# Optimization experiments

Hardware: AMD Instinct MI355X
Metric: run time of the kernel (lower is better)

The kernel has to match this reference:

```python
import jax, jax.numpy as jnp
import numpy as np

NUM_ITERS = 5
EPS = 1e-5


def setup_inputs() -> dict:
    key = jax.random.key(0)
    ks = jax.random.split(key, 5)
    C_in, C_out, D, H, W = 64, 64, 64, 256, 256
    return {
        "x": jax.random.normal(ks[0], (C_in, H, W), dtype=jnp.float32),
        "conv_w": jax.random.normal(ks[1], (C_out, C_in, 3, 3), dtype=jnp.float32) * 0.05,
        "conv_b": jax.random.normal(ks[2], (C_out,), dtype=jnp.float32) * 0.05,
        "bin_proj": jax.random.normal(ks[3], (C_out, D, 1), dtype=jnp.float32),
        "weight_matrix": jax.random.normal(ks[4], (C_out, D, D), dtype=jnp.float32),
        "gn_weight": jnp.ones((C_out,), dtype=jnp.float32),
        "gn_bias": jnp.zeros((C_out,), dtype=jnp.float32),
    }


def reference(x, conv_w, conv_b, bin_proj, weight_matrix, gn_weight, gn_bias):
    # query conv: (C_in,H,W) -> (C_out,H,W), SAME padding
    q = jax.lax.conv_general_dilated(
        x[None], conv_w, window_strides=(1, 1), padding="SAME",
        dimension_numbers=("NCHW", "OIHW", "NCHW"))[0]
    q = q + conv_b[:, None, None]

    bp = bin_proj[:, :, 0]  # (C, D) == bin_proj_c[:, 0] per channel
    # binary query / initial state: (C, H, W, D)
    state = jnp.sign(q[:, :, :, None] * bp[:, None, None, :])
    # unrolled Hopfield dynamics: state = sign(W_c @ state) per channel/pixel
    for _ in range(NUM_ITERS):
        state = jnp.sign(jnp.einsum("cde,chwe->chwd", weight_matrix, state))
    # readout: sum_d bp[c,d] * state[c,h,w,d] -> (C,H,W)
    out = jnp.einsum("cd,chwd->chw", bp, state)

    # GroupNorm(groups=1) over (C,H,W) with per-channel affine, then residual input is out+q
    y = out + q
    mean = jnp.mean(y)
    var = jnp.mean(jnp.square(y - mean))
    yn = (y - mean) * jax.lax.rsqrt(var + EPS)
    yn = yn * gn_weight[:, None, None] + gn_bias[:, None, None]
    return jax.nn.gelu(yn)
```

## Files before the change

kernel.cpp:

```cpp
#include <hip/hip_runtime.h>
#include <math.h>

#define N_TOT 4194304
#define CONV_BLOCKS 1024
#define XS_PAD 4864

__device__ __forceinline__ float sgnf(float x) {
    return x > 0.f ? 1.f : (x < 0.f ? -1.f : 0.f);
}

__device__ __forceinline__ float gelu_f(float v) {
    const float c0 = 0.7978845608028654f;
    float inner = c0 * fmaf(0.044715f * v, v * v, v);
    return 0.5f * v * (1.f + tanhf(inner));
}

__device__ __forceinline__ void gll4(const float* g, float* l) {
    __builtin_amdgcn_global_load_lds((const __attribute__((address_space(1))) void*)g,
                                     (__attribute__((address_space(3))) void*)l, 4, 0, 0);
}

__global__ __launch_bounds__(64) void alpha_kernel(const float* __restrict__ bp,
                                                   const float* __restrict__ Wm,
                                                   float* __restrict__ alpha) {
    const int c = blockIdx.x, d = threadIdx.x;
    __shared__ float v[64];
    float bpv = bp[c * 64 + d];
    v[d] = sgnf(bpv);
    __syncthreads();
    const float* row = Wm + c * 4096 + d * 64;
    for (int it = 0; it < 5; ++it) {
        float s = 0.f;
        #pragma unroll
        for (int e = 0; e < 64; ++e) s = fmaf(row[e], v[e], s);
        __syncthreads();
        v[d] = sgnf(s);
        __syncthreads();
    }
    float val = bpv * v[d];
    #pragma unroll
    for (int off = 32; off; off >>= 1) val += __shfl_down(val, off);
    if (d == 0) alpha[c] = val;
}

#define LOAD_T(T, XSC, CIOFF)                                                 \
    {                                                                         \
        _Pragma("unroll")                                                     \
        for (int rr = 0; rr < 4; ++rr) {                                      \
            const int off_ = lrow + rr * 136 + (CIOFF);                       \
            float2 a_ = *reinterpret_cast<const float2*>(&(XSC)[off_]);       \
            float2 b_ = *reinterpret_cast<const float2*>(&(XSC)[off_ + 2]);   \
            T[rr][0] = a_.x; T[rr][1] = a_.y; T[rr][2] = b_.x; T[rr][3] = b_.y;\
        }                                                                     \
    }

#define FMA_CI(T, WP)                                                         \
    {                                                                         \
        _Pragma("unroll")                                                     \
        for (int co = 0; co < 4; ++co) {                                      \
            const float* w_ = (WP) + co * 576;                                \
            _Pragma("unroll")                                                 \
            for (int ky = 0; ky < 3; ++ky)                                    \
                _Pragma("unroll")                                             \
                for (int kx = 0; kx < 3; ++kx) {                              \
                    float wv_ = w_[ky * 3 + kx];                              \
                    _Pragma("unroll")                                         \
                    for (int dy = 0; dy < 2; ++dy)                            \
                        _Pragma("unroll")                                     \
                        for (int j = 0; j < 2; ++j)                           \
                            acc[co][dy][j] = fmaf(wv_, T[dy + ky][kx + j],    \
                                                  acc[co][dy][j]);            \
                }                                                             \
        }                                                                     \
    }

__global__ __launch_bounds__(256, 2) void conv_kernel(const float* __restrict__ x,
                                                      const float* __restrict__ cw,
                                                      const float* __restrict__ cb,
                                                      const float* __restrict__ alpha,
                                                      const float* __restrict__ zbuf,
                                                      float* __restrict__ y,
                                                      double* __restrict__ partials) {
    const int tid = threadIdx.x;
    const int b = blockIdx.x;
    const int tile = b & 63;
    const int cog = b >> 6;
    const int bx = tile & 7, by = tile >> 3;
    const int tx = tid & 15, ty = tid >> 4;

    __shared__ float xs[2][XS_PAD];
    __shared__ double red[4][2];

    int voff[19];
    unsigned vmask = 0u;
    #pragma unroll
    for (int i = 0; i < 19; ++i) {
        int idx = i * 256 + tid;
        int r = idx / 136;
        int rem = idx - r * 136;
        int ci = rem / 34;
        int c = rem - ci * 34;
        int gy = (by << 5) - 1 + r;
        int gx = (bx << 5) + c - 1;
        bool ok = (idx < 4624) && ((unsigned)gy < 256u) && ((unsigned)gx < 256u);
        voff[i] = (ci << 16) + (gy << 8) + gx;
        if (ok) vmask |= (1u << i);
    }

    float acc[4][2][2];
    #pragma unroll
    for (int co = 0; co < 4; ++co) {
        float bias = cb[cog * 4 + co];
        acc[co][0][0] = bias; acc[co][0][1] = bias;
        acc[co][1][0] = bias; acc[co][1][1] = bias;
    }

    #pragma unroll
    for (int i = 0; i < 19; ++i) {
        const float* src = (vmask & (1u << i)) ? (x + voff[i]) : zbuf;
        gll4(src, &xs[0][i * 256 + tid]);
    }
    __syncthreads();

    const int lrow = (2 * ty) * 136 + 2 * tx;
    const float* wbase = cw + cog * 4 * 576;

    float tA[4][4], tB[4][4];

    for (int s = 0; s < 16; ++s) {
        const int cur = s & 1;
        if (s < 15) {
            const float* xb = x + ((s + 1) << 18);
            #pragma unroll
            for (int i = 0; i < 19; ++i) {
                const float* src = (vmask & (1u << i)) ? (xb + voff[i]) : zbuf;
                gll4(src, &xs[cur ^ 1][i * 256 + tid]);
            }
        }

        const float* xsc = xs[cur];
        const float* wp = wbase + (s * 4) * 9;

        LOAD_T(tA, xsc, 0)
        LOAD_T(tB, xsc, 34)
        FMA_CI(tA, wp)
        LOAD_T(tA, xsc, 68)
        FMA_CI(tB, wp + 9)
        LOAD_T(tB, xsc, 102)
        FMA_CI(tA, wp + 18)
        FMA_CI(tB, wp + 27)

        __syncthreads();
    }

    double s1 = 0.0, s2 = 0.0;
    const int gx0 = (bx << 5) + 2 * tx;
    const int gy0 = (by << 5) + 2 * ty;
    #pragma unroll
    for (int co = 0; co < 4; ++co) {
        float a = alpha[cog * 4 + co];
        const int cb_off = (cog * 4 + co) << 16;
        #pragma unroll
        for (int dy = 0; dy < 2; ++dy) {
            float q0 = acc[co][dy][0];
            float q1 = acc[co][dy][1];
            float y0v = q0 + (q0 > 0.f ? a : (q0 < 0.f ? -a : 0.f));
            float y1v = q1 + (q1 > 0.f ? a : (q1 < 0.f ? -a : 0.f));
            float2 pk; pk.x = y0v; pk.y = y1v;
            *reinterpret_cast<float2*>(&y[cb_off + ((gy0 + dy) << 8) + gx0]) = pk;
            s1 += (double)y0v + (double)y1v;
            s2 += (double)y0v * (double)y0v + (double)y1v * (double)y1v;
        }
    }
    #pragma unroll
    for (int off = 32; off; off >>= 1) {
        s1 += __shfl_down(s1, off);
        s2 += __shfl_down(s2, off);
    }
    const int wid = tid >> 6;
    if ((tid & 63) == 0) { red[wid][0] = s1; red[wid][1] = s2; }
    __syncthreads();
    if (tid == 0) {
        double a1 = red[0][0] + red[1][0] + red[2][0] + red[3][0];
        double a2 = red[0][1] + red[1][1] + red[2][1] + red[3][1];
        partials[b * 2]     = a1;
        partials[b * 2 + 1] = a2;
    }
}

__global__ __launch_bounds__(256) void stats_kernel(const double* __restrict__ partials,
                                                    float* __restrict__ stats) {
    const int tid = threadIdx.x;
    double s1 = 0.0, s2 = 0.0;
    for (int i = tid; i < CONV_BLOCKS; i += 256) {
        s1 += partials[2 * i];
        s2 += partials[2 * i + 1];
    }
    #pragma unroll
    for (int off = 32; off; off >>= 1) {
        s1 += __shfl_down(s1, off);
        s2 += __shfl_down(s2, off);
    }
    __shared__ double red[4][2];
    const int wid = tid >> 6;
    if ((tid & 63) == 0) { red[wid][0] = s1; red[wid][1] = s2; }
    __syncthreads();
    if (tid == 0) {
        double a1 = red[0][0] + red[1][0] + red[2][0] + red[3][0];
        double a2 = red[0][1] + red[1][1] + red[2][1] + red[3][1];
        double mean = a1 / (double)N_TOT;
        double var = a2 / (double)N_TOT - mean * mean;
        stats[0] = (float)mean;
        stats[1] = (float)(1.0 / sqrt(var + 1e-5));
    }
}

__global__ __launch_bounds__(256) void finalize_kernel(float* __restrict__ y,
                                                       const float* __restrict__ stats,
                                                       const float* __restrict__ gnw,
                                                       const float* __restrict__ gnb) {
    const int i = blockIdx.x * 256 + threadIdx.x;
    const float mean = stats[0], istd = stats[1];
    const int c = i >> 14;
    const float scale = gnw[c] * istd;
    const float shift = gnb[c] - mean * scale;
    float4 v = reinterpret_cast<float4*>(y)[i];
    v.x = gelu_f(fmaf(v.x, scale, shift));
    v.y = gelu_f(fmaf(v.y, scale, shift));
    v.z = gelu_f(fmaf(v.z, scale, shift));
    v.w = gelu_f(fmaf(v.w, scale, shift));
    reinterpret_cast<float4*>(y)[i] = v;
}

extern "C" void kernel_launch(void* const* d_in, const int* in_sizes, int n_in,
                              void* d_out, int out_size, void* d_ws, size_t ws_size,
                              hipStream_t stream) {
    const float* x   = (const float*)d_in[0];
    const float* cw  = (const float*)d_in[1];
    const float* cb  = (const float*)d_in[2];
    const float* bp  = (const float*)d_in[3];
    const float* Wm  = (const float*)d_in[4];
    const float* gnw = (const float*)d_in[5];
    const float* gnb = (const float*)d_in[6];
    float* out = (float*)d_out;

    char* ws = (char*)d_ws;
    float* alpha     = (float*)ws;
    float* stats     = (float*)(ws + 256);
    double* partials = (double*)(ws + 512);
    float* zbuf      = (float*)(ws + 32768);

    hipMemsetAsync(zbuf, 0, 256, stream);
    alpha_kernel<<<64, 64, 0, stream>>>(bp, Wm, alpha);
    conv_kernel<<<CONV_BLOCKS, 256, 0, stream>>>(x, cw, cb, alpha, zbuf, out, partials);
    stats_kernel<<<1, 256, 0, stream>>>(partials, stats);
    finalize_kernel<<<4096, 256, 0, stream>>>(out, stats, gnw, gnb);
}
```

Measured before the change: 101.1 us.

## Pre-pad input into workspace so conv tiles load with 16-byte global-to-LDS copies

Adds a pad_kernel that writes a zero-padded, pitch-aligned copy of x (258 rows by 272 columns per channel) into the workspace. The conv kernel then stages each tile with 5 16-byte global_load_lds ops per thread instead of 19 4-byte ones, with no per-element bounds masks. The LDS tile stride changes to 144 and the reduction scratch is aliased into the tile buffer. It costs an extra pass over the input (about 18 MB written) plus a kernel launch, and it falls back to the old kernel when the workspace is too small.

```diff
diff --git a/kernel.cpp b/kernel.cpp
--- a/kernel.cpp
+++ b/kernel.cpp
@@ -3,7 +3,13 @@
 
 #define N_TOT 4194304
 #define CONV_BLOCKS 1024
-#define XS_PAD 4864
+#define XS_DW 5120
+#define PITCH 272
+#define PROWS 258
+#define PCI (PROWS * PITCH)
+#define PAD_TOT (64 * PCI)
+#define PAD_BYTES (PAD_TOT * 4)
+#define WS_PAD_OFF 32768
 
 __device__ __forceinline__ float sgnf(float x) {
     return x > 0.f ? 1.f : (x < 0.f ? -1.f : 0.f);
@@ -18,6 +24,10 @@
 __device__ __forceinline__ void gll4(const float* g, float* l) {
     __builtin_amdgcn_global_load_lds((const __attribute__((address_space(1))) void*)g,
                                      (__attribute__((address_space(3))) void*)l, 4, 0, 0);
+}
+__device__ __forceinline__ void gll16(const float* g, float* l) {
+    __builtin_amdgcn_global_load_lds((const __attribute__((address_space(1))) void*)g,
+                                     (__attribute__((address_space(3))) void*)l, 16, 0, 0);
 }
 
 __global__ __launch_bounds__(64) void alpha_kernel(const float* __restrict__ bp,
@@ -43,11 +53,24 @@
     if (d == 0) alpha[c] = val;
 }
 
+__global__ __launch_bounds__(256) void pad_kernel(const float* __restrict__ x,
+                                                  float* __restrict__ pad) {
+    const int idx = blockIdx.x * 256 + threadIdx.x;
+    const int ci = idx / PCI;
+    int rem = idx - ci * PCI;
+    const int py = rem / PITCH;
+    const int px = rem - py * PITCH;
+    float v = 0.f;
+    if (py >= 1 && py <= 256 && px >= 1 && px <= 256)
+        v = x[(ci << 16) + ((py - 1) << 8) + (px - 1)];
+    pad[idx] = v;
+}
+
 #define LOAD_T(T, XSC, CIOFF)                                                 \
     {                                                                         \
         _Pragma("unroll")                                                     \
         for (int rr = 0; rr < 4; ++rr) {                                      \
-            const int off_ = lrow + rr * 136 + (CIOFF);                       \
+            const int off_ = lrow + rr * 144 + (CIOFF);                       \
             float2 a_ = *reinterpret_cast<const float2*>(&(XSC)[off_]);       \
             float2 b_ = *reinterpret_cast<const float2*>(&(XSC)[off_ + 2]);   \
             T[rr][0] = a_.x; T[rr][1] = a_.y; T[rr][2] = b_.x; T[rr][3] = b_.y;\
@@ -74,11 +97,10 @@
         }                                                                     \
     }
 
-__global__ __launch_bounds__(256, 2) void conv_kernel(const float* __restrict__ x,
+__global__ __launch_bounds__(256, 2) void conv_kernel(const float* __restrict__ xp,
                                                       const float* __restrict__ cw,
                                                       const float* __restrict__ cb,
                                                       const float* __restrict__ alpha,
-                                                      const float* __restrict__ zbuf,
                                                       float* __restrict__ y,
                                                       double* __restrict__ partials) {
     const int tid = threadIdx.x;
@@ -88,23 +110,19 @@
     const int bx = tile & 7, by = tile >> 3;
     const int tx = tid & 15, ty = tid >> 4;
 
-    __shared__ float xs[2][XS_PAD];
-    __shared__ double red[4][2];
-
-    int voff[19];
-    unsigned vmask = 0u;
-    #pragma unroll
-    for (int i = 0; i < 19; ++i) {
-        int idx = i * 256 + tid;
-        int r = idx / 136;
-        int rem = idx - r * 136;
-        int ci = rem / 34;
-        int c = rem - ci * 34;
-        int gy = (by << 5) - 1 + r;
-        int gx = (bx << 5) + c - 1;
-        bool ok = (idx < 4624) && ((unsigned)gy < 256u) && ((unsigned)gx < 256u);
-        voff[i] = (ci << 16) + (gy << 8) + gx;
-        if (ok) vmask |= (1u << i);
+    __shared__ float xs[2][XS_DW];
+    double* red = (double*)&xs[1][4896];
+
+    int goff[5];
+    #pragma unroll
+    for (int i = 0; i < 5; ++i) {
+        int c4 = i * 256 + tid;
+        int r = c4 / 36;
+        int rem = c4 - r * 36;
+        int ci = rem / 9;
+        int cc = rem - ci * 9;
+        int g = ci * PCI + ((by << 5) + r) * PITCH + (bx << 5) + cc * 4;
+        goff[i] = (c4 < 1224) ? g : 0;
     }
 
     float acc[4][2][2];
@@ -116,13 +134,11 @@
     }
 
     #pragma unroll
-    for (int i = 0; i < 19; ++i) {
-        const float* src = (vmask & (1u << i)) ? (x + voff[i]) : zbuf;
-        gll4(src, &xs[0][i * 256 + tid]);
-    }
-    __syncthreads();
-
-    const int lrow = (2 * ty) * 136 + 2 * tx;
+    for (int i = 0; i < 5; ++i)
+        gll16(xp + goff[i], &xs[0][(i * 256 + tid) * 4]);
+    __syncthreads();
+
+    const int lrow = (2 * ty) * 144 + 2 * tx;
     const float* wbase = cw + cog * 4 * 576;
 
     float tA[4][4], tB[4][4];
@@ -130,23 +146,21 @@
     for (int s = 0; s < 16; ++s) {
         const int cur = s & 1;
         if (s < 15) {
-            const float* xb = x + ((s + 1) << 18);
+            const float* xb = xp + (s + 1) * (4 * PCI);
             #pragma unroll
-            for (int i = 0; i < 19; ++i) {
-                const float* src = (vmask & (1u << i)) ? (xb + voff[i]) : zbuf;
-                gll4(src, &xs[cur ^ 1][i * 256 + tid]);
-            }
+            for (int i = 0; i < 5; ++i)
+                gll16(xb + goff[i], &xs[cur ^ 1][(i * 256 + tid) * 4]);
         }
 
         const float* xsc = xs[cur];
         const float* wp = wbase + (s * 4) * 9;
 
         LOAD_T(tA, xsc, 0)
-        LOAD_T(tB, xsc, 34)
+        LOAD_T(tB, xsc, 36)
         FMA_CI(tA, wp)
-        LOAD_T(tA, xsc, 68)
+        LOAD_T(tA, xsc, 72)
         FMA_CI(tB, wp + 9)
-        LOAD_T(tB, xsc, 102)
+        LOAD_T(tB, xsc, 108)
         FMA_CI(tA, wp + 18)
         FMA_CI(tB, wp + 27)
 
@@ -178,13 +192,138 @@
         s2 += __shfl_down(s2, off);
     }
     const int wid = tid >> 6;
-    if ((tid & 63) == 0) { red[wid][0] = s1; red[wid][1] = s2; }
+    if ((tid & 63) == 0) { red[wid * 2] = s1; red[wid * 2 + 1] = s2; }
     __syncthreads();
     if (tid == 0) {
-        double a1 = red[0][0] + red[1][0] + red[2][0] + red[3][0];
-        double a2 = red[0][1] + red[1][1] + red[2][1] + red[3][1];
+        double a1 = red[0] + red[2] + red[4] + red[6];
+        double a2 = red[1] + red[3] + red[5] + red[7];
         partials[b * 2]     = a1;
         partials[b * 2 + 1] = a2;
+    }
+}
+
+__global__ __launch_bounds__(256, 2) void conv_fb(const float* __restrict__ x,
+                                                  const float* __restrict__ cw,
+                                                  const float* __restrict__ cb,
+                                                  const float* __restrict__ alpha,
+                                                  const float* __restrict__ zbuf,
+                                                  float* __restrict__ y,
+                                                  double* __restrict__ partials) {
+    const int tid = threadIdx.x;
+    const int b = blockIdx.x;
+    const int tile = b & 63;
+    const int cog = b >> 6;
+    const int bx = tile & 7, by = tile >> 3;
+    const int tx = tid & 15, ty = tid >> 4;
+
+    __shared__ float xs[2][4864];
+    __shared__ double red[4][2];
+
+    int voff[19];
+    unsigned vmask = 0u;
+    #pragma unroll
+    for (int i = 0; i < 19; ++i) {
+        int idx = i * 256 + tid;
+        int r = idx / 136;
+        int rem = idx - r * 136;
+        int ci = rem / 34;
+        int c = rem - ci * 34;
+        int gy = (by << 5) - 1 + r;
+        int gx = (bx << 5) + c - 1;
+        bool ok = (idx < 4624) && ((unsigned)gy < 256u) && ((unsigned)gx < 256u);
+        voff[i] = (ci << 16) + (gy << 8) + gx;
+        if (ok) vmask |= (1u << i);
+    }
+
+    float acc[4][2][2];
+    #pragma unroll
+    for (int co = 0; co < 4; ++co) {
+        float bias = cb[cog * 4 + co];
+        acc[co][0][0] = bias; acc[co][0][1] = bias;
+        acc[co][1][0] = bias; acc[co][1][1] = bias;
+    }
+
+    #pragma unroll
+    for (int i = 0; i < 19; ++i) {
+        const float* src = (vmask & (1u << i)) ? (x + voff[i]) : zbuf;
+        gll4(src, &xs[0][i * 256 + tid]);
+    }
+    __syncthreads();
+
+    const int lrow2 = (2 * ty) * 136 + 2 * tx;
+    const float* wbase = cw + cog * 4 * 576;
+
+    for (int s = 0; s < 16; ++s) {
+        const int cur = s & 1;
+        if (s < 15) {
+            const float* xb = x + ((s + 1) << 18);
+            #pragma unroll
+            for (int i = 0; i < 19; ++i) {
+                const float* src = (vmask & (1u << i)) ? (xb + voff[i]) : zbuf;
+                gll4(src, &xs[cur ^ 1][i * 256 + tid]);
+            }
+        }
+        const float* xsc = xs[cur];
+        #pragma unroll
+        for (int ci = 0; ci < 4; ++ci) {
+            float t[4][4];
+            #pragma unroll
+            for (int rr = 0; rr < 4; ++rr) {
+                const int off = lrow2 + rr * 136 + ci * 34;
+                float2 a = *reinterpret_cast<const float2*>(&xsc[off]);
+                float2 bb = *reinterpret_cast<const float2*>(&xsc[off + 2]);
+                t[rr][0] = a.x; t[rr][1] = a.y; t[rr][2] = bb.x; t[rr][3] = bb.y;
+            }
+            const float* wp = wbase + (s * 4 + ci) * 9;
+            #pragma unroll
+            for (int co = 0; co < 4; ++co) {
+                const float* w = wp + co * 576;
+                #pragma unroll
+                for (int ky = 0; ky < 3; ++ky)
+                    #pragma unroll
+                    for (int kx = 0; kx < 3; ++kx) {
+                        float wv = w[ky * 3 + kx];
+                        #pragma unroll
+                        for (int dy = 0; dy < 2; ++dy)
+                            #pragma unroll
+                            for (int j = 0; j < 2; ++j)
+                                acc[co][dy][j] = fmaf(wv, t[dy + ky][kx + j], acc[co][dy][j]);
+                    }
+            }
+        }
+        __syncthreads();
+    }
+
+    double s1 = 0.0, s2 = 0.0;
+    const int gx0 = (bx << 5) + 2 * tx;
+    const int gy0 = (by << 5) + 2 * ty;
+    #pragma unroll
+    for (int co = 0; co < 4; ++co) {
+        float a = alpha[cog * 4 + co];
+        const int cb_off = (cog * 4 + co) << 16;
+        #pragma unroll
+        for (int dy = 0; dy < 2; ++dy) {
+            float q0 = acc[co][dy][0];
+            float q1 = acc[co][dy][1];
+            float y0v = q0 + (q0 > 0.f ? a : (q0 < 0.f ? -a : 0.f));
+            float y1v = q1 + (q1 > 0.f ? a : (q1 < 0.f ? -a : 0.f));
+            float2 pk; pk.x = y0v; pk.y = y1v;
+            *reinterpret_cast<float2*>(&y[cb_off + ((gy0 + dy) << 8) + gx0]) = pk;
+            s1 += (double)y0v + (double)y1v;
+            s2 += (double)y0v * (double)y0v + (double)y1v * (double)y1v;
+        }
+    }
+    #pragma unroll
+    for (int off = 32; off; off >>= 1) {
+        s1 += __shfl_down(s1, off);
+        s2 += __shfl_down(s2, off);
+    }
+    const int wid = tid >> 6;
+    if ((tid & 63) == 0) { red[wid][0] = s1; red[wid][1] = s2; }
+    __syncthreads();
+    if (tid == 0) {
+        partials[b * 2]     = red[0][0] + red[1][0] + red[2][0] + red[3][0];
+        partials[b * 2 + 1] = red[0][1] + red[1][1] + red[2][1] + red[3][1];
     }
 }
 
@@ -248,11 +387,19 @@
     float* alpha     = (float*)ws;
     float* stats     = (float*)(ws + 256);
     double* partials = (double*)(ws + 512);
-    float* zbuf      = (float*)(ws + 32768);
-
-    hipMemsetAsync(zbuf, 0, 256, stream);
+
     alpha_kernel<<<64, 64, 0, stream>>>(bp, Wm, alpha);
-    conv_kernel<<<CONV_BLOCKS, 256, 0, stream>>>(x, cw, cb, alpha, zbuf, out, partials);
+
+    if (ws_size >= (size_t)WS_PAD_OFF + PAD_BYTES) {
+        float* xpad = (float*)(ws + WS_PAD_OFF);
+        pad_kernel<<<PAD_TOT / 256, 256, 0, stream>>>(x, xpad);
+        conv_kernel<<<CONV_BLOCKS, 256, 0, stream>>>(xpad, cw, cb, alpha, out, partials);
+    } else {
+        float* zbuf = (float*)(ws + 32768);
+        hipMemsetAsync(zbuf, 0, 256, stream);
+        conv_fb<<<CONV_BLOCKS, 256, 0, stream>>>(x, cw, cb, alpha, zbuf, out, partials);
+    }
+
     stats_kernel<<<1, 256, 0, stream>>>(partials, stats);
     finalize_kernel<<<4096, 256, 0, stream>>>(out, stats, gnw, gnb);
 }
```

Result: faster. 91.58 us (-9.4%).
